# Kernel optimization log

Measured on AMD Instinct MI355X. Metric: run time of the kernel, lower is better.

## Reference

```python
import jax, jax.numpy as jnp
import numpy as np

B, C, N, T = 32, 32, 300, 64      # batch, residual/conv channels, nodes, seq_len
DIM, K, SKIP, GD = 40, 20, 64, 2  # node_dim, top-k (subgraph_size), skip_channels, gcn_depth
TANH_A, PROP_A = 3.0, 0.05
KSET = (2, 3, 6, 7)
TOUT = T - (KSET[-1] - 1)          # 58: time length after dilated inception (dilation=1)


def conv2d(x, w, b):
    y = jax.lax.conv_general_dilated(x, w, (1, 1), 'VALID', dimension_numbers=('NCHW', 'OIHW', 'NCHW'))
    return y + b[None, :, None, None]


def setup_inputs() -> dict:
    key = jax.random.key(0)
    ks = iter(jax.random.split(key, 48))
    def nrm(shape, s=1.0):
        return jax.random.normal(next(ks), shape, jnp.float32) * s
    inp = {
        'x': nrm((B, C, N, T)),
        'x_skip': nrm((B, SKIP, N, 1)),
        'idx': jnp.arange(N, dtype=jnp.int32),
        'emb1': nrm((N, DIM), 0.1), 'emb2': nrm((N, DIM), 0.1),
        'lin1_w': nrm((DIM, DIM), 0.15), 'lin1_b': jnp.zeros((DIM,), jnp.float32),
        'lin2_w': nrm((DIM, DIM), 0.15), 'lin2_b': jnp.zeros((DIM,), jnp.float32),
        'skip_w': nrm((SKIP, C, 1, TOUT), 0.05), 'skip_b': jnp.zeros((SKIP,), jnp.float32),
        'mp1_w': nrm((C, (GD + 1) * C, 1, 1), 0.1), 'mp1_b': jnp.zeros((C,), jnp.float32),
        'mp2_w': nrm((C, (GD + 1) * C, 1, 1), 0.1), 'mp2_b': jnp.zeros((C,), jnp.float32),
        'ln_w': jnp.ones((C, N, TOUT), jnp.float32), 'ln_b': jnp.zeros((C, N, TOUT), jnp.float32),
    }
    for k in KSET:
        inp[f'fw{k}'] = nrm((C // 4, C, 1, k), 0.1); inp[f'fb{k}'] = jnp.zeros((C // 4,), jnp.float32)
        inp[f'gw{k}'] = nrm((C // 4, C, 1, k), 0.1); inp[f'gb{k}'] = jnp.zeros((C // 4,), jnp.float32)
    return inp


def _forward(x, x_skip, idx, emb1, emb2, lin1_w, lin1_b, lin2_w, lin2_b,
             fws, gws, skip_w, skip_b, mp1_w, mp1_b, mp2_w, mp2_b, ln_w, ln_b):
    # --- GraphConstructor: learned sparse adjacency via tanh/relu/top-k/scatter ---
    n1 = jnp.tanh(TANH_A * (emb1[idx] @ lin1_w.T + lin1_b))
    n2 = jnp.tanh(TANH_A * (emb2[idx] @ lin2_w.T + lin2_b))
    a = n1 @ n2.T - n2 @ n1.T
    A = jax.nn.relu(jnp.tanh(TANH_A * a))
    _, cols = jax.lax.top_k(A, K)                               # [N, K] per-row top-k indices
    mask = jnp.zeros_like(A).at[jnp.arange(N)[:, None], cols].set(1.0)
    A = A * mask
    # --- DilatedInception filter/gate (Conv2d kernel (1,k), crop to shortest) ---
    Xf = jnp.tanh(jnp.concatenate([conv2d(x, w, b)[..., -TOUT:] for w, b in fws], axis=1))
    Xg = jax.nn.sigmoid(jnp.concatenate([conv2d(x, w, b)[..., -TOUT:] for w, b in gws], axis=1))
    X = Xf * Xg                                                 # dropout is identity (training=False)
    X_skip_out = conv2d(X, skip_w, skip_b) + x_skip             # [B, SKIP, N, 1]
    # --- MixProp graph diffusion over A and A^T ---
    def mixprop(Xin, Adj, w, b):
        Ah = Adj + jnp.eye(N, dtype=Adj.dtype)
        Ah = Ah / Ah.sum(1)[:, None]                            # row-normalize
        H, hops = Xin, [Xin]
        for _ in range(GD):
            H = PROP_A * Xin + (1.0 - PROP_A) * jnp.einsum('bcwt,vw->bcvt', H, Ah)
            hops.append(H)
        return conv2d(jnp.concatenate(hops, axis=1), w, b)      # 1x1 conv: (GD+1)*C -> C
    X = mixprop(X, A, mp1_w, mp1_b) + mixprop(X, A.T, mp2_w, mp2_b)
    X = X + x[..., -TOUT:]
    # --- LayerNorm over (C, N, TOUT) with node-indexed affine ---
    mu = X.mean(axis=(1, 2, 3), keepdims=True)
    var = ((X - mu) ** 2).mean(axis=(1, 2, 3), keepdims=True)
    Xn = (X - mu) * jax.lax.rsqrt(var + 1e-5)
    X = Xn * ln_w[:, idx, :][None] + ln_b[:, idx, :][None]
    return X, X_skip_out


def reference(x, x_skip, idx, emb1, emb2, lin1_w, lin1_b, lin2_w, lin2_b,
              fw2, fb2, fw3, fb3, fw6, fb6, fw7, fb7,
              gw2, gb2, gw3, gb3, gw6, gb6, gw7, gb7,
              skip_w, skip_b, mp1_w, mp1_b, mp2_w, mp2_b, ln_w, ln_b):
    fws = [(fw2, fb2), (fw3, fb3), (fw6, fb6), (fw7, fb7)]
    gws = [(gw2, gb2), (gw3, gb3), (gw6, gb6), (gw7, gb7)]
    return _forward(x, x_skip, idx, emb1, emb2, lin1_w, lin1_b, lin2_w, lin2_b,
                    fws, gws, skip_w, skip_b, mp1_w, mp1_b, mp2_w, mp2_b, ln_w, ln_b)
```

## Files before the change

kernel.cpp:

```cpp
#include <hip/hip_runtime.h>
#include <hip/hip_bf16.h>
#include <math.h>

typedef __hip_bfloat16 bf16;
typedef __attribute__((ext_vector_type(8))) short bf16x8;
typedef __attribute__((ext_vector_type(4))) float f32x4;

#define NB 32
#define NC 32
#define NNODE 300
#define NT 64
#define NDIM 40
#define KTOP 20
#define NSKIP 64
#define NTOUT 58
#define SLAB 17400
#define BSLAB 556800
#define XEL 17817600
#define PSLAB 2048
#define BPSLAB 614400
#define XPEL 19660800

__device__ __forceinline__ float b2f(bf16 v){ return __bfloat162float(v); }
__device__ __forceinline__ bf16 f2b(float v){ return __float2bfloat16(v); }
__device__ __forceinline__ float fsig(float x){ return 1.0f/(1.0f + __expf(-x)); }
__device__ __forceinline__ float ftanh(float x){ return 2.0f*fsig(2.0f*x) - 1.0f; }

__device__ __forceinline__ unsigned short bbits(float v){
  bf16 h = f2b(v); unsigned short s; __builtin_memcpy(&s, &h, 2); return s;
}

__device__ __forceinline__ void fma8(float acc[8], uint4 d, float vv){
  acc[0] = fmaf(vv, __uint_as_float(d.x << 16),          acc[0]);
  acc[1] = fmaf(vv, __uint_as_float(d.x & 0xffff0000u),  acc[1]);
  acc[2] = fmaf(vv, __uint_as_float(d.y << 16),          acc[2]);
  acc[3] = fmaf(vv, __uint_as_float(d.y & 0xffff0000u),  acc[3]);
  acc[4] = fmaf(vv, __uint_as_float(d.z << 16),          acc[4]);
  acc[5] = fmaf(vv, __uint_as_float(d.z & 0xffff0000u),  acc[5]);
  acc[6] = fmaf(vv, __uint_as_float(d.w << 16),          acc[6]);
  acc[7] = fmaf(vv, __uint_as_float(d.w & 0xffff0000u),  acc[7]);
}

__device__ __forceinline__ void unp8(float f[8], uint4 d){
  f[0] = __uint_as_float(d.x << 16); f[1] = __uint_as_float(d.x & 0xffff0000u);
  f[2] = __uint_as_float(d.y << 16); f[3] = __uint_as_float(d.y & 0xffff0000u);
  f[4] = __uint_as_float(d.z << 16); f[5] = __uint_as_float(d.z & 0xffff0000u);
  f[6] = __uint_as_float(d.w << 16); f[7] = __uint_as_float(d.w & 0xffff0000u);
}

__device__ __forceinline__ uint4 pack8(const float f[8]){
  uint4 d;
  d.x = (unsigned)bbits(f[0]) | ((unsigned)bbits(f[1]) << 16);
  d.y = (unsigned)bbits(f[2]) | ((unsigned)bbits(f[3]) << 16);
  d.z = (unsigned)bbits(f[4]) | ((unsigned)bbits(f[5]) << 16);
  d.w = (unsigned)bbits(f[6]) | ((unsigned)bbits(f[7]) << 16);
  return d;
}

__device__ __forceinline__ void bv_swz(int bid, int& b, int& v){
  int xcd = bid & 7, i = bid >> 3;
  int nb = xcd*1200 + i;
  b = nb / NNODE; v = nb - b*NNODE;
}

__global__ void k_nodes(const float* __restrict__ emb1, const float* __restrict__ emb2,
                        const float* __restrict__ l1w, const float* __restrict__ l1b,
                        const float* __restrict__ l2w, const float* __restrict__ l2b,
                        const int* __restrict__ idxp,
                        float* __restrict__ n1, float* __restrict__ n2){
  int i = blockIdx.x; int d = threadIdx.x;
  if (d >= NDIM) return;
  int r = idxp[i];
  float a1 = l1b[d], a2 = l2b[d];
  for (int k=0;k<NDIM;++k){
    a1 = fmaf(emb1[r*NDIM+k], l1w[d*NDIM+k], a1);
    a2 = fmaf(emb2[r*NDIM+k], l2w[d*NDIM+k], a2);
  }
  n1[i*NDIM+d] = tanhf(3.0f*a1);
  n2[i*NDIM+d] = tanhf(3.0f*a2);
}

__global__ void __launch_bounds__(64) k_adjrow(const float* __restrict__ n1,
                                               const float* __restrict__ n2,
                                               float* __restrict__ Am){
  int i = blockIdx.x; int lane = threadIdx.x;
  __shared__ float rowo[NNODE];
  __shared__ float rowv[NNODE];
  __shared__ int   sel[NNODE];
  for (int j=lane;j<NNODE;j+=64){
    float a = 0.f;
    #pragma unroll
    for (int k=0;k<NDIM;++k){
      float a1 = n1[i*NDIM+k], a2 = n2[i*NDIM+k];
      a = fmaf(a1, n2[j*NDIM+k], a);
      a = fmaf(-a2, n1[j*NDIM+k], a);
    }
    float v = tanhf(3.0f*a);
    v = v > 0.f ? v : 0.f;
    rowo[j]=v; rowv[j]=v; sel[j]=0;
  }
  __syncthreads();
  for (int it=0; it<KTOP; ++it){
    float best = -1.f; int bi = 0x7fffffff;
    for (int j=lane;j<NNODE;j+=64){
      float v = rowv[j];
      if (v > best){ best=v; bi=j; }
    }
    #pragma unroll
    for (int off=32; off; off>>=1){
      float ov = __shfl_xor(best, off);
      int   oi = __shfl_xor(bi, off);
      if (ov > best || (ov == best && oi < bi)){ best=ov; bi=oi; }
    }
    if (lane==0){ sel[bi]=1; rowv[bi]=-2.f; }
    __syncthreads();
  }
  for (int j=lane;j<NNODE;j+=64)
    Am[i*NNODE+j] = sel[j] ? rowo[j] : 0.f;
}

__global__ void __launch_bounds__(64) k_csr(const float* __restrict__ Am,
                                            int* __restrict__ aidx, float* __restrict__ aval,
                                            int* __restrict__ acnt){
  int r = blockIdx.x; int lane = threadIdx.x;
  int v = (r < NNODE) ? r : r - NNODE;
  int*   ip = aidx + r*304;
  float* vp = aval + r*304;
  if (lane==0){ ip[0]=v; vp[0]=1.0f; }
  int cnt = 1; float s = 1.0f;
  for (int base=0; base<NNODE; base+=64){
    int j = base + lane; float val = 0.f; bool p = false;
    if (j < NNODE){
      val = (r < NNODE) ? Am[v*NNODE + j] : Am[j*NNODE + v];
      p = val > 0.f;
    }
    unsigned long long m = __ballot(p);
    int pre = __popcll(m & ((1ull << lane) - 1ull));
    if (p){ ip[cnt+pre]=j; vp[cnt+pre]=val; }
    cnt += __popcll(m);
    float vs = p ? val : 0.f;
    #pragma unroll
    for (int off=32; off; off>>=1) vs += __shfl_xor(vs, off);
    s += vs;
  }
  for (int e=lane; e<cnt; e+=64) vp[e] = vp[e] / s;
  if (lane==0) acnt[r]=cnt;
}

__global__ void k_wpack2(const float* __restrict__ fw2,const float* __restrict__ fw3,
                         const float* __restrict__ fw6,const float* __restrict__ fw7,
                         const float* __restrict__ gw2,const float* __restrict__ gw3,
                         const float* __restrict__ gw6,const float* __restrict__ gw7,
                         const float* __restrict__ fb2,const float* __restrict__ fb3,
                         const float* __restrict__ fb6,const float* __restrict__ fb7,
                         const float* __restrict__ gb2,const float* __restrict__ gb3,
                         const float* __restrict__ gb6,const float* __restrict__ gb7,
                         bf16* __restrict__ wfA, float* __restrict__ biasPk){
  int T = blockIdx.x*blockDim.x + threadIdx.x;
  if (T < 14336){
    int j = T & 7;
    int q = T >> 3;
    int l = q & 63; q >>= 6;
    int ks = q % 7, mt = q / 7;
    int m = mt*16 + (l & 15);
    int k = ks*32 + (l >> 4)*8 + j;
    int c = m >> 1, path = m & 1;
    int cls = c >> 3, o = c & 7;
    int ic = k / 7, d = k - ic*7;
    int kk = (cls==0) ? 2 : (cls==1) ? 3 : (cls==2) ? 6 : 7;
    int tp = d - (7 - kk);
    float val = 0.f;
    if (tp >= 0){
      const float* w = (path==0)
        ? (cls==0?fw2:cls==1?fw3:cls==2?fw6:fw7)
        : (cls==0?gw2:cls==1?gw3:cls==2?gw6:gw7);
      val = w[(o*NC + ic)*kk + tp];
    }
    wfA[T] = f2b(val);
  } else if (T < 14336 + 32){
    int c = T - 14336;
    int cls = c >> 3, o = c & 7;
    const float* fb = cls==0?fb2:cls==1?fb3:cls==2?fb6:fb7;
    const float* gb = cls==0?gb2:cls==1?gb3:cls==2?gb6:gb7;
    biasPk[c*2]   = fb[o];
    biasPk[c*2+1] = gb[o];
  }
}

__global__ void k_wprepM(const float* __restrict__ m1w, const float* __restrict__ m2w,
                         const float* __restrict__ m1b, const float* __restrict__ m2b,
                         bf16* __restrict__ pkB0, bf16* __restrict__ pkB1,
                         float* __restrict__ biasSum){
  int id = blockIdx.x*blockDim.x + threadIdx.x;
  if (id < 3072){
    int j = id & 7, l = (id >> 3) & 63, q = id >> 9;
    int ks = q % 3, nt = q / 3;
    int k = ks*32 + (l >> 4)*8 + j;
    int c = nt*16 + (l & 15);
    float val = m1w[c*96 + k] + (k < 32 ? m2w[c*96 + k] : 0.f);
    pkB0[id] = f2b(val);
  } else if (id < 5120){
    int id2 = id - 3072;
    int j = id2 & 7, l = (id2 >> 3) & 63, q = id2 >> 9;
    int ks = q & 1, nt = q >> 1;
    int k = ks*32 + (l >> 4)*8 + j;
    int c = nt*16 + (l & 15);
    pkB1[id2] = f2b(m2w[c*96 + 32 + k]);
  } else if (id < 5152){
    int c = id - 5120;
    biasSum[c] = m1b[c] + m2b[c];
  }
}

__global__ void k_wTb(const float* __restrict__ sw, bf16* __restrict__ wTb){
  int id = blockIdx.x*blockDim.x + threadIdx.x;
  if (id >= 131072) return;
  int j = id & 7, l = (id >> 3) & 63, q = id >> 9;
  int ks = q & 63, nt = q >> 6;
  int k = ks*32 + (l >> 4)*8 + j;
  int t = k >> 5, c = k & 31;
  int sc = nt*16 + (l & 15);
  float val = (t < NTOUT) ? sw[sc*1856 + c*NTOUT + t] : 0.f;
  wTb[id] = f2b(val);
}

__global__ void __launch_bounds__(256) k_incepM(const float* __restrict__ x,
    const bf16* __restrict__ wfA, const float* __restrict__ biasPk,
    bf16* __restrict__ Xp){
  __shared__ bf16 xsb[32*72];
  __shared__ uint4 xim2[28*64];
  int b, n; bv_swz(blockIdx.x, b, n);
  int bn = b*NNODE + n;
  int tid = threadIdx.x;
  {
    int c = tid >> 3, t0 = (tid & 7)*8;
    const float* src = x + ((size_t)(b*NC + c)*NNODE + n)*NT + t0;
    float4 v0 = *reinterpret_cast<const float4*>(src);
    float4 v1 = *reinterpret_cast<const float4*>(src + 4);
    float f[8] = {v0.x,v0.y,v0.z,v0.w,v1.x,v1.y,v1.z,v1.w};
    *reinterpret_cast<uint4*>(&xsb[c*72 + t0]) = pack8(f);
    if ((tid & 7) == 7)
      *reinterpret_cast<uint4*>(&xsb[c*72 + 64]) = make_uint4(0,0,0,0);
  }
  __syncthreads();
  #pragma unroll
  for (int i=0;i<7;++i){
    int pr = tid + i*256;
    int kb = pr >> 6, t = pr & 63;
    int k0 = kb*8;
    int ic = k0 / 7, d = k0 - ic*7;
    unsigned sh[8];
    #pragma unroll
    for (int j=0;j<8;++j){
      sh[j] = *reinterpret_cast<const unsigned short*>(&xsb[ic*72 + t + d]);
      ++d; if (d == 7){ d = 0; ++ic; }
    }
    xim2[kb*64 + t] = make_uint4(sh[0]|(sh[1]<<16), sh[2]|(sh[3]<<16),
                                 sh[4]|(sh[5]<<16), sh[6]|(sh[7]<<16));
  }
  __syncthreads();
  int lane = tid & 63;
  int mt = __builtin_amdgcn_readfirstlane(tid >> 6);
  bf16x8 wA[7];
  #pragma unroll
  for (int ks=0; ks<7; ++ks)
    wA[ks] = *reinterpret_cast<const bf16x8*>(wfA + (size_t)((mt*7 + ks)*64 + lane)*8);
  int g = lane >> 4;
  int c0 = mt*8 + 2*g;
  float4 bias2 = *reinterpret_cast<const float4*>(biasPk + c0*2);
  #pragma unroll
  for (int nt=0; nt<4; ++nt){
    int t = (lane & 15) + nt*16;
    f32x4 acc = {0.f, 0.f, 0.f, 0.f};
    #pragma unroll
    for (int ks=0; ks<7; ++ks){
      bf16x8 bfr = __builtin_bit_cast(bf16x8, xim2[(ks*4 + g)*64 + t]);
      acc = __builtin_amdgcn_mfma_f32_16x16x32_bf16(wA[ks], bfr, acc, 0, 0, 0);
    }
    bool act = t < NTOUT;
    float X0 = act ? (ftanh(acc[0] + bias2.x) * fsig(acc[1] + bias2.y)) : 0.f;
    float X1 = act ? (ftanh(acc[2] + bias2.z) * fsig(acc[3] + bias2.w)) : 0.f;
    unsigned pv = (unsigned)bbits(X0) | ((unsigned)bbits(X1) << 16);
    *reinterpret_cast<unsigned*>(Xp + (size_t)bn*PSLAB + t*32 + c0) = pv;
  }
}

__global__ void __launch_bounds__(256) k_skipM(const bf16* __restrict__ Xp, const bf16* __restrict__ wTb,
      const float* __restrict__ skip_b, const float* __restrict__ x_skip, float* __restrict__ out){
  int bn0 = blockIdx.x * 16;
  int tid = threadIdx.x, lane = tid & 63;
  int nt = __builtin_amdgcn_readfirstlane(tid >> 6);
  int g = lane >> 4, col = lane & 15;
  const bf16* aptr = Xp + (size_t)(bn0 + col)*PSLAB + g*8;
  const bf16* bptr = wTb + ((size_t)nt*64*64 + lane)*8;
  f32x4 acc = {0.f, 0.f, 0.f, 0.f};
  #pragma unroll 4
  for (int ks=0; ks<64; ++ks){
    bf16x8 aF = *reinterpret_cast<const bf16x8*>(aptr + ks*32);
    bf16x8 bF = *reinterpret_cast<const bf16x8*>(bptr + (size_t)ks*512);
    acc = __builtin_amdgcn_mfma_f32_16x16x32_bf16(aF, bF, acc, 0, 0, 0);
  }
  int sc = nt*16 + col;
  float sb = skip_b[sc];
  #pragma unroll
  for (int r=0;r<4;++r){
    int bn = bn0 + g*4 + r;
    int b = bn / NNODE, n = bn - b*NNODE;
    size_t so = (size_t)b*NSKIP*NNODE + (size_t)sc*NNODE + n;
    out[(size_t)XEL + so] = acc[r] + sb + x_skip[so];
  }
}

__global__ void __launch_bounds__(256) k_prop(const bf16* __restrict__ Xp, bf16* __restrict__ HA,
    const int* __restrict__ aidx, const float* __restrict__ aval, const int* __restrict__ acnt,
    int rowoff){
  __shared__ int   sidx[304];
  __shared__ float sval[304];
  int b, v; bv_swz(blockIdx.x, b, v);
  int r = rowoff + v;
  int cnt = acnt[r];
  for (int e = threadIdx.x; e < cnt; e += 256){
    sidx[e] = aidx[r*304 + e] * PSLAB;
    sval[e] = aval[r*304 + e];
  }
  __syncthreads();
  int t = threadIdx.x >> 2, cb = threadIdx.x & 3;
  int off = t*32 + cb*8;
  const bf16* base = Xp + (size_t)b*BPSLAB + off;
  float acc[8] = {0,0,0,0,0,0,0,0};
  #pragma unroll 2
  for (int j=0;j<cnt;++j){
    uint4 d = *reinterpret_cast<const uint4*>(base + sidx[j]);
    fma8(acc, d, sval[j]);
  }
  size_t own = (size_t)b*BPSLAB + (size_t)v*PSLAB + off;
  uint4 dx = *reinterpret_cast<const uint4*>(Xp + own);
  float xf[8]; unp8(xf, dx);
  float h[8];
  #pragma unroll
  for (int k=0;k<8;++k) h[k] = fmaf(0.95f, acc[k], 0.05f*xf[k]);
  *reinterpret_cast<uint4*>(HA + own) = pack8(h);
}

__global__ void __launch_bounds__(256) k_fuse(const bf16* __restrict__ Xp, const bf16* __restrict__ HA,
    float* __restrict__ out, const float* __restrict__ x,
    const int* __restrict__ aidx, const float* __restrict__ aval, const int* __restrict__ acnt,
    const bf16* __restrict__ pkB, const float* __restrict__ biasSum,
    int rowoff, int side){
  __shared__ int   sidx[304];
  __shared__ float sval[304];
  __shared__ uint4 h2T4[256];
  int b, v; bv_swz(blockIdx.x, b, v);
  int r = rowoff + v;
  int cnt = acnt[r];
  for (int e = threadIdx.x; e < cnt; e += 256){
    sidx[e] = aidx[r*304 + e] * PSLAB;
    sval[e] = aval[r*304 + e];
  }
  __syncthreads();
  int tid = threadIdx.x;
  size_t bbase = (size_t)b*BPSLAB;
  size_t vbase = bbase + (size_t)v*PSLAB;
  {
    int t = tid >> 2, cb = tid & 3;
    int off = t*32 + cb*8;
    const bf16* base = HA + bbase + off;
    float acc[8] = {0,0,0,0,0,0,0,0};
    #pragma unroll 2
    for (int j=0;j<cnt;++j){
      uint4 d = *reinterpret_cast<const uint4*>(base + sidx[j]);
      fma8(acc, d, sval[j]);
    }
    uint4 dx = *reinterpret_cast<const uint4*>(Xp + vbase + off);
    float xf[8]; unp8(xf, dx);
    float h[8];
    #pragma unroll
    for (int k=0;k<8;++k) h[k] = fmaf(0.95f, acc[k], 0.05f*xf[k]);
    h2T4[t*4 + cb] = pack8(h);
  }
  __syncthreads();
  int lane = tid & 63;
  int mt = __builtin_amdgcn_readfirstlane(tid >> 6);
  int g = lane >> 4, col = lane & 15;
  int tRow = mt*16 + col;
  const bf16x8* h2p = reinterpret_cast<const bf16x8*>(h2T4);
  bf16x8 aF0, aF1, aF2;
  if (side == 0){
    aF0 = *reinterpret_cast<const bf16x8*>(Xp + vbase + tRow*32 + g*8);
    aF1 = *reinterpret_cast<const bf16x8*>(HA + vbase + tRow*32 + g*8);
    aF2 = h2p[tRow*4 + g];
  } else {
    aF0 = *reinterpret_cast<const bf16x8*>(HA + vbase + tRow*32 + g*8);
    aF1 = h2p[tRow*4 + g];
    aF2 = aF1;
  }
  int t0 = mt*16 + g*4;
  #pragma unroll
  for (int nt=0; nt<2; ++nt){
    int c_out = nt*16 + col;
    f32x4 acc;
    if (side == 0){
      float bv = biasSum[c_out];
      acc = (f32x4){bv, bv, bv, bv};
      bf16x8 w0 = *reinterpret_cast<const bf16x8*>(pkB + (size_t)((nt*3+0)*64 + lane)*8);
      bf16x8 w1 = *reinterpret_cast<const bf16x8*>(pkB + (size_t)((nt*3+1)*64 + lane)*8);
      bf16x8 w2 = *reinterpret_cast<const bf16x8*>(pkB + (size_t)((nt*3+2)*64 + lane)*8);
      acc = __builtin_amdgcn_mfma_f32_16x16x32_bf16(aF0, w0, acc, 0, 0, 0);
      acc = __builtin_amdgcn_mfma_f32_16x16x32_bf16(aF1, w1, acc, 0, 0, 0);
      acc = __builtin_amdgcn_mfma_f32_16x16x32_bf16(aF2, w2, acc, 0, 0, 0);
      float* po = out + ((size_t)(b*NC + c_out)*NNODE + v)*NTOUT + t0;
      if (t0 <= 54){
        *reinterpret_cast<float2*>(po)     = make_float2(acc[0], acc[1]);
        *reinterpret_cast<float2*>(po + 2) = make_float2(acc[2], acc[3]);
      } else if (t0 == 56){
        *reinterpret_cast<float2*>(po)     = make_float2(acc[0], acc[1]);
      }
    } else {
      acc = (f32x4){0.f, 0.f, 0.f, 0.f};
      bf16x8 w0 = *reinterpret_cast<const bf16x8*>(pkB + (size_t)((nt*2+0)*64 + lane)*8);
      bf16x8 w1 = *reinterpret_cast<const bf16x8*>(pkB + (size_t)((nt*2+1)*64 + lane)*8);
      acc = __builtin_amdgcn_mfma_f32_16x16x32_bf16(aF0, w0, acc, 0, 0, 0);
      acc = __builtin_amdgcn_mfma_f32_16x16x32_bf16(aF1, w1, acc, 0, 0, 0);
      float* po = out + ((size_t)(b*NC + c_out)*NNODE + v)*NTOUT + t0;
      const float* rx = x + ((size_t)(b*NC + c_out)*NNODE + v)*NT + 6 + t0;
      if (t0 <= 54){
        float2 o0 = *reinterpret_cast<const float2*>(po);
        float2 o1 = *reinterpret_cast<const float2*>(po + 2);
        float2 r0 = *reinterpret_cast<const float2*>(rx);
        float2 r1 = *reinterpret_cast<const float2*>(rx + 2);
        *reinterpret_cast<float2*>(po)     = make_float2(o0.x + acc[0] + r0.x, o0.y + acc[1] + r0.y);
        *reinterpret_cast<float2*>(po + 2) = make_float2(o1.x + acc[2] + r1.x, o1.y + acc[3] + r1.y);
      } else if (t0 == 56){
        float2 o0 = *reinterpret_cast<const float2*>(po);
        float2 r0 = *reinterpret_cast<const float2*>(rx);
        *reinterpret_cast<float2*>(po)     = make_float2(o0.x + acc[0] + r0.x, o0.y + acc[1] + r0.y);
      }
    }
  }
}

__global__ void __launch_bounds__(256) k_lnstat(const float* __restrict__ out, double* __restrict__ part){
  int blk = blockIdx.x; int b = blk >> 3, seg = blk & 7;
  const float* p = out + (size_t)b*BSLAB;
  int start = seg*69600, end = start + 69600;
  double s = 0.0, s2 = 0.0;
  for (int i = start + threadIdx.x; i < end; i += 256){
    double v = (double)p[i]; s += v; s2 += v*v;
  }
  #pragma unroll
  for (int off=32; off; off>>=1){ s += __shfl_down(s, off); s2 += __shfl_down(s2, off); }
  __shared__ double ls[4], ls2[4];
  int lane = threadIdx.x & 63, w = threadIdx.x >> 6;
  if (lane==0){ ls[w]=s; ls2[w]=s2; }
  __syncthreads();
  if (threadIdx.x==0){
    double a=0.0, a2=0.0;
    for (int i=0;i<4;++i){ a+=ls[i]; a2+=ls2[i]; }
    part[blk*2]=a; part[blk*2+1]=a2;
  }
}

__global__ void k_lnfin(const double* __restrict__ part, float* __restrict__ stats){
  int b = threadIdx.x; if (b >= 32) return;
  double s=0.0, s2=0.0;
  for (int seg=0; seg<8; ++seg){ s += part[(b*8+seg)*2]; s2 += part[(b*8+seg)*2+1]; }
  double n = (double)BSLAB;
  double mean = s/n;
  double var = s2/n - mean*mean;
  stats[b*2]   = (float)mean;
  stats[b*2+1] = (float)(1.0/sqrt(var + 1e-5));
}

__global__ void __launch_bounds__(256) k_lnapply(float* __restrict__ out, const float* __restrict__ stats,
        const float* __restrict__ lnw, const float* __restrict__ lnb, const int* __restrict__ idxp){
  int o = blockIdx.x*256 + threadIdx.x;
  int t = o % NTOUT; int v = (o / NTOUT) % NNODE; int c = (o / SLAB) % NC; int b = o / BSLAB;
  float mean = stats[b*2], rstd = stats[b*2+1];
  int vn = idxp[v];
  float wv = lnw[((size_t)c*NNODE + vn)*NTOUT + t];
  float bv = lnb[((size_t)c*NNODE + vn)*NTOUT + t];
  float vx = out[o];
  out[o] = (vx - mean)*rstd*wv + bv;
}

extern "C" void kernel_launch(void* const* d_in, const int* in_sizes, int n_in,
                              void* d_out, int out_size, void* d_ws, size_t ws_size,
                              hipStream_t stream) {
  (void)in_sizes; (void)n_in; (void)out_size; (void)ws_size;
  const float* x     = (const float*)d_in[0];
  const float* xskip = (const float*)d_in[1];
  const int*   idxp  = (const int*)d_in[2];
  const float* emb1  = (const float*)d_in[3];
  const float* emb2  = (const float*)d_in[4];
  const float* l1w   = (const float*)d_in[5];
  const float* l1b   = (const float*)d_in[6];
  const float* l2w   = (const float*)d_in[7];
  const float* l2b   = (const float*)d_in[8];
  const float* skw   = (const float*)d_in[9];
  const float* skb   = (const float*)d_in[10];
  const float* m1w   = (const float*)d_in[11];
  const float* m1b   = (const float*)d_in[12];
  const float* m2w   = (const float*)d_in[13];
  const float* m2b   = (const float*)d_in[14];
  const float* lnw   = (const float*)d_in[15];
  const float* lnb   = (const float*)d_in[16];
  const float* fw2=(const float*)d_in[17]; const float* fb2=(const float*)d_in[18];
  const float* gw2=(const float*)d_in[19]; const float* gb2=(const float*)d_in[20];
  const float* fw3=(const float*)d_in[21]; const float* fb3=(const float*)d_in[22];
  const float* gw3=(const float*)d_in[23]; const float* gb3=(const float*)d_in[24];
  const float* fw6=(const float*)d_in[25]; const float* fb6=(const float*)d_in[26];
  const float* gw6=(const float*)d_in[27]; const float* gb6=(const float*)d_in[28];
  const float* fw7=(const float*)d_in[29]; const float* fb7=(const float*)d_in[30];
  const float* gw7=(const float*)d_in[31]; const float* gb7=(const float*)d_in[32];
  float* out = (float*)d_out;

  char* wsbase = (char*)d_ws;
  size_t cur = 0;
  auto alloc = [&](size_t bytes)->char*{
    char* p = wsbase + cur;
    cur = (cur + bytes + 255) & ~(size_t)255;
    return p;
  };
  bf16*  Xp   = (bf16*) alloc((size_t)XPEL*2);
  bf16*  HA   = (bf16*) alloc((size_t)XPEL*2);
  float* n1   = (float*)alloc(12000*4);
  float* n2   = (float*)alloc(12000*4);
  float* Am   = (float*)alloc(90000*4);
  int*   aidx = (int*)  alloc(600*304*4);
  float* aval = (float*)alloc(600*304*4);
  int*   acnt = (int*)  alloc(600*4);
  bf16*  wTb  = (bf16*) alloc(131072*2);
  bf16*  wfA  = (bf16*) alloc(14336*2);
  float* biasPk = (float*)alloc(64*4);
  bf16*  pkB0 = (bf16*) alloc(3072*2);
  bf16*  pkB1 = (bf16*) alloc(2048*2);
  float* biasSum = (float*)alloc(32*4);
  double* part = (double*)alloc(256*2*8);
  float* stats = (float*)alloc(64*4);

  k_nodes <<<NNODE, 64, 0, stream>>>(emb1, emb2, l1w, l1b, l2w, l2b, idxp, n1, n2);
  k_adjrow<<<NNODE, 64, 0, stream>>>(n1, n2, Am);
  k_csr   <<<2*NNODE, 64, 0, stream>>>(Am, aidx, aval, acnt);

  k_wpack2<<<57, 256, 0, stream>>>(fw2,fw3,fw6,fw7, gw2,gw3,gw6,gw7,
                                   fb2,fb3,fb6,fb7, gb2,gb3,gb6,gb7, wfA, biasPk);
  k_wprepM<<<21, 256, 0, stream>>>(m1w, m2w, m1b, m2b, pkB0, pkB1, biasSum);
  k_wTb   <<<512, 256, 0, stream>>>(skw, wTb);

  k_incepM<<<NB*NNODE, 256, 0, stream>>>(x, wfA, biasPk, Xp);

  k_skipM<<<(NB*NNODE)/16, 256, 0, stream>>>(Xp, wTb, skb, xskip, out);

  k_prop<<<NB*NNODE, 256, 0, stream>>>(Xp, HA, aidx, aval, acnt, 0);
  k_fuse<<<NB*NNODE, 256, 0, stream>>>(Xp, HA, out, x, aidx, aval, acnt, pkB0, biasSum, 0, 0);

  k_prop<<<NB*NNODE, 256, 0, stream>>>(Xp, HA, aidx, aval, acnt, NNODE);
  k_fuse<<<NB*NNODE, 256, 0, stream>>>(Xp, HA, out, x, aidx, aval, acnt, pkB1, biasSum, NNODE, 1);

  k_lnstat<<<256, 256, 0, stream>>>(out, part);
  k_lnfin<<<1, 32, 0, stream>>>(part, stats);
  k_lnapply<<<XEL/256, 256, 0, stream>>>(out, stats, lnw, lnb, idxp);
}
```

Measured before the change: 454.6 us.

## Merge both mixprop sides into one prop launch and one fused MFMA epilogue

Runs the first-hop propagation for A and A^T in a single k_prop launch writing to separate HA buffers, with an XCD-aware block mapping. A single k_fuse kernel then does the second hop for both sides, stages X and all hops in padded shared memory, and applies a combined 5-slice MFMA 1x1 conv with a repacked weight buffer. The output is written once, which removes the read-modify-write of out and two kernel launches. In exchange it needs an extra HA buffer, more shared memory per block, and doubles the gather work inside each fuse block.

```diff
diff --git a/kernel.cpp b/kernel.cpp
--- a/kernel.cpp
+++ b/kernel.cpp
@@ -189,23 +189,20 @@
 
 __global__ void k_wprepM(const float* __restrict__ m1w, const float* __restrict__ m2w,
                          const float* __restrict__ m1b, const float* __restrict__ m2b,
-                         bf16* __restrict__ pkB0, bf16* __restrict__ pkB1,
-                         float* __restrict__ biasSum){
+                         bf16* __restrict__ pkB, float* __restrict__ biasSum){
   int id = blockIdx.x*blockDim.x + threadIdx.x;
-  if (id < 3072){
+  if (id < 5120){
     int j = id & 7, l = (id >> 3) & 63, q = id >> 9;
-    int ks = q % 3, nt = q / 3;
-    int k = ks*32 + (l >> 4)*8 + j;
+    int ks = q % 5, nt = q / 5;
+    int k = (l >> 4)*8 + j;
     int c = nt*16 + (l & 15);
-    float val = m1w[c*96 + k] + (k < 32 ? m2w[c*96 + k] : 0.f);
-    pkB0[id] = f2b(val);
-  } else if (id < 5120){
-    int id2 = id - 3072;
-    int j = id2 & 7, l = (id2 >> 3) & 63, q = id2 >> 9;
-    int ks = q & 1, nt = q >> 1;
-    int k = ks*32 + (l >> 4)*8 + j;
-    int c = nt*16 + (l & 15);
-    pkB1[id2] = f2b(m2w[c*96 + 32 + k]);
+    float val;
+    if      (ks == 0) val = m1w[c*96 + k] + m2w[c*96 + k];
+    else if (ks == 1) val = m1w[c*96 + 32 + k];
+    else if (ks == 2) val = m1w[c*96 + 64 + k];
+    else if (ks == 3) val = m2w[c*96 + 32 + k];
+    else              val = m2w[c*96 + 64 + k];
+    pkB[id] = f2b(val);
   } else if (id < 5152){
     int c = id - 5120;
     biasSum[c] = m1b[c] + m2b[c];
@@ -311,13 +308,18 @@
   }
 }
 
-__global__ void __launch_bounds__(256) k_prop(const bf16* __restrict__ Xp, bf16* __restrict__ HA,
-    const int* __restrict__ aidx, const float* __restrict__ aval, const int* __restrict__ acnt,
-    int rowoff){
+__global__ void __launch_bounds__(256) k_prop(const bf16* __restrict__ Xp,
+    bf16* __restrict__ HA0, bf16* __restrict__ HA1,
+    const int* __restrict__ aidx, const float* __restrict__ aval, const int* __restrict__ acnt){
   __shared__ int   sidx[304];
   __shared__ float sval[304];
-  int b, v; bv_swz(blockIdx.x, b, v);
-  int r = rowoff + v;
+  int bid = blockIdx.x;
+  int xcd = bid & 7, i = bid >> 3;
+  int side = i & 1, jj = i >> 1;
+  int nb = xcd*1200 + jj;
+  int b = nb / NNODE, v = nb - b*NNODE;
+  int r = (side ? NNODE : 0) + v;
+  bf16* HA = side ? HA1 : HA0;
   int cnt = acnt[r];
   for (int e = threadIdx.x; e < cnt; e += 256){
     sidx[e] = aidx[r*304 + e] * PSLAB;
@@ -328,7 +330,7 @@
   int off = t*32 + cb*8;
   const bf16* base = Xp + (size_t)b*BPSLAB + off;
   float acc[8] = {0,0,0,0,0,0,0,0};
-  #pragma unroll 2
+  #pragma unroll 4
   for (int j=0;j<cnt;++j){
     uint4 d = *reinterpret_cast<const uint4*>(base + sidx[j]);
     fma8(acc, d, sval[j]);
@@ -342,99 +344,106 @@
   *reinterpret_cast<uint4*>(HA + own) = pack8(h);
 }
 
-__global__ void __launch_bounds__(256) k_fuse(const bf16* __restrict__ Xp, const bf16* __restrict__ HA,
+__global__ void __launch_bounds__(256) k_fuse(const bf16* __restrict__ Xp,
+    const bf16* __restrict__ HA0, const bf16* __restrict__ HA1,
     float* __restrict__ out, const float* __restrict__ x,
     const int* __restrict__ aidx, const float* __restrict__ aval, const int* __restrict__ acnt,
-    const bf16* __restrict__ pkB, const float* __restrict__ biasSum,
-    int rowoff, int side){
-  __shared__ int   sidx[304];
-  __shared__ float sval[304];
-  __shared__ uint4 h2T4[256];
+    const bf16* __restrict__ pkB, const float* __restrict__ biasSum){
+  __shared__ int   sidx0[304];
+  __shared__ float sval0[304];
+  __shared__ int   sidx1[304];
+  __shared__ float sval1[304];
+  __shared__ uint4 xs4[320];
+  __shared__ uint4 h1a4[320];
+  __shared__ uint4 h2a4[320];
+  __shared__ uint4 h1b4[320];
+  __shared__ uint4 h2b4[320];
   int b, v; bv_swz(blockIdx.x, b, v);
-  int r = rowoff + v;
-  int cnt = acnt[r];
-  for (int e = threadIdx.x; e < cnt; e += 256){
-    sidx[e] = aidx[r*304 + e] * PSLAB;
-    sval[e] = aval[r*304 + e];
+  int r0 = v, r1 = NNODE + v;
+  int cnt0 = acnt[r0], cnt1 = acnt[r1];
+  for (int e = threadIdx.x; e < cnt0; e += 256){
+    sidx0[e] = aidx[r0*304 + e] * PSLAB;
+    sval0[e] = aval[r0*304 + e];
+  }
+  for (int e = threadIdx.x; e < cnt1; e += 256){
+    sidx1[e] = aidx[r1*304 + e] * PSLAB;
+    sval1[e] = aval[r1*304 + e];
   }
   __syncthreads();
   int tid = threadIdx.x;
+  int t = tid >> 2, cb = tid & 3;
+  int off = t*32 + cb*8;
+  int idx = t*5 + cb;
   size_t bbase = (size_t)b*BPSLAB;
   size_t vbase = bbase + (size_t)v*PSLAB;
+  uint4 dx = *reinterpret_cast<const uint4*>(Xp + vbase + off);
+  xs4[idx] = dx;
+  float xf[8]; unp8(xf, dx);
+  h1a4[idx] = *reinterpret_cast<const uint4*>(HA0 + vbase + off);
+  h1b4[idx] = *reinterpret_cast<const uint4*>(HA1 + vbase + off);
   {
-    int t = tid >> 2, cb = tid & 3;
-    int off = t*32 + cb*8;
-    const bf16* base = HA + bbase + off;
+    const bf16* base = HA0 + bbase + off;
     float acc[8] = {0,0,0,0,0,0,0,0};
-    #pragma unroll 2
-    for (int j=0;j<cnt;++j){
-      uint4 d = *reinterpret_cast<const uint4*>(base + sidx[j]);
-      fma8(acc, d, sval[j]);
-    }
-    uint4 dx = *reinterpret_cast<const uint4*>(Xp + vbase + off);
-    float xf[8]; unp8(xf, dx);
+    #pragma unroll 4
+    for (int j=0;j<cnt0;++j){
+      uint4 d = *reinterpret_cast<const uint4*>(base + sidx0[j]);
+      fma8(acc, d, sval0[j]);
+    }
     float h[8];
     #pragma unroll
     for (int k=0;k<8;++k) h[k] = fmaf(0.95f, acc[k], 0.05f*xf[k]);
-    h2T4[t*4 + cb] = pack8(h);
+    h2a4[idx] = pack8(h);
+  }
+  {
+    const bf16* base = HA1 + bbase + off;
+    float acc[8] = {0,0,0,0,0,0,0,0};
+    #pragma unroll 4
+    for (int j=0;j<cnt1;++j){
+      uint4 d = *reinterpret_cast<const uint4*>(base + sidx1[j]);
+      fma8(acc, d, sval1[j]);
+    }
+    float h[8];
+    #pragma unroll
+    for (int k=0;k<8;++k) h[k] = fmaf(0.95f, acc[k], 0.05f*xf[k]);
+    h2b4[idx] = pack8(h);
   }
   __syncthreads();
   int lane = tid & 63;
   int mt = __builtin_amdgcn_readfirstlane(tid >> 6);
   int g = lane >> 4, col = lane & 15;
   int tRow = mt*16 + col;
-  const bf16x8* h2p = reinterpret_cast<const bf16x8*>(h2T4);
-  bf16x8 aF0, aF1, aF2;
-  if (side == 0){
-    aF0 = *reinterpret_cast<const bf16x8*>(Xp + vbase + tRow*32 + g*8);
-    aF1 = *reinterpret_cast<const bf16x8*>(HA + vbase + tRow*32 + g*8);
-    aF2 = h2p[tRow*4 + g];
-  } else {
-    aF0 = *reinterpret_cast<const bf16x8*>(HA + vbase + tRow*32 + g*8);
-    aF1 = h2p[tRow*4 + g];
-    aF2 = aF1;
-  }
+  int fidx = tRow*5 + g;
+  bf16x8 aX  = __builtin_bit_cast(bf16x8, xs4[fidx]);
+  bf16x8 a1a = __builtin_bit_cast(bf16x8, h1a4[fidx]);
+  bf16x8 a2a = __builtin_bit_cast(bf16x8, h2a4[fidx]);
+  bf16x8 a1b = __builtin_bit_cast(bf16x8, h1b4[fidx]);
+  bf16x8 a2b = __builtin_bit_cast(bf16x8, h2b4[fidx]);
   int t0 = mt*16 + g*4;
   #pragma unroll
   for (int nt=0; nt<2; ++nt){
     int c_out = nt*16 + col;
-    f32x4 acc;
-    if (side == 0){
-      float bv = biasSum[c_out];
-      acc = (f32x4){bv, bv, bv, bv};
-      bf16x8 w0 = *reinterpret_cast<const bf16x8*>(pkB + (size_t)((nt*3+0)*64 + lane)*8);
-      bf16x8 w1 = *reinterpret_cast<const bf16x8*>(pkB + (size_t)((nt*3+1)*64 + lane)*8);
-      bf16x8 w2 = *reinterpret_cast<const bf16x8*>(pkB + (size_t)((nt*3+2)*64 + lane)*8);
-      acc = __builtin_amdgcn_mfma_f32_16x16x32_bf16(aF0, w0, acc, 0, 0, 0);
-      acc = __builtin_amdgcn_mfma_f32_16x16x32_bf16(aF1, w1, acc, 0, 0, 0);
-      acc = __builtin_amdgcn_mfma_f32_16x16x32_bf16(aF2, w2, acc, 0, 0, 0);
-      float* po = out + ((size_t)(b*NC + c_out)*NNODE + v)*NTOUT + t0;
-      if (t0 <= 54){
-        *reinterpret_cast<float2*>(po)     = make_float2(acc[0], acc[1]);
-        *reinterpret_cast<float2*>(po + 2) = make_float2(acc[2], acc[3]);
-      } else if (t0 == 56){
-        *reinterpret_cast<float2*>(po)     = make_float2(acc[0], acc[1]);
-      }
-    } else {
-      acc = (f32x4){0.f, 0.f, 0.f, 0.f};
-      bf16x8 w0 = *reinterpret_cast<const bf16x8*>(pkB + (size_t)((nt*2+0)*64 + lane)*8);
-      bf16x8 w1 = *reinterpret_cast<const bf16x8*>(pkB + (size_t)((nt*2+1)*64 + lane)*8);
-      acc = __builtin_amdgcn_mfma_f32_16x16x32_bf16(aF0, w0, acc, 0, 0, 0);
-      acc = __builtin_amdgcn_mfma_f32_16x16x32_bf16(aF1, w1, acc, 0, 0, 0);
-      float* po = out + ((size_t)(b*NC + c_out)*NNODE + v)*NTOUT + t0;
-      const float* rx = x + ((size_t)(b*NC + c_out)*NNODE + v)*NT + 6 + t0;
-      if (t0 <= 54){
-        float2 o0 = *reinterpret_cast<const float2*>(po);
-        float2 o1 = *reinterpret_cast<const float2*>(po + 2);
-        float2 r0 = *reinterpret_cast<const float2*>(rx);
-        float2 r1 = *reinterpret_cast<const float2*>(rx + 2);
-        *reinterpret_cast<float2*>(po)     = make_float2(o0.x + acc[0] + r0.x, o0.y + acc[1] + r0.y);
-        *reinterpret_cast<float2*>(po + 2) = make_float2(o1.x + acc[2] + r1.x, o1.y + acc[3] + r1.y);
-      } else if (t0 == 56){
-        float2 o0 = *reinterpret_cast<const float2*>(po);
-        float2 r0 = *reinterpret_cast<const float2*>(rx);
-        *reinterpret_cast<float2*>(po)     = make_float2(o0.x + acc[0] + r0.x, o0.y + acc[1] + r0.y);
-      }
+    float bv = biasSum[c_out];
+    f32x4 acc = {bv, bv, bv, bv};
+    bf16x8 w0 = *reinterpret_cast<const bf16x8*>(pkB + (size_t)((nt*5+0)*64 + lane)*8);
+    bf16x8 w1 = *reinterpret_cast<const bf16x8*>(pkB + (size_t)((nt*5+1)*64 + lane)*8);
+    bf16x8 w2 = *reinterpret_cast<const bf16x8*>(pkB + (size_t)((nt*5+2)*64 + lane)*8);
+    bf16x8 w3 = *reinterpret_cast<const bf16x8*>(pkB + (size_t)((nt*5+3)*64 + lane)*8);
+    bf16x8 w4 = *reinterpret_cast<const bf16x8*>(pkB + (size_t)((nt*5+4)*64 + lane)*8);
+    acc = __builtin_amdgcn_mfma_f32_16x16x32_bf16(aX,  w0, acc, 0, 0, 0);
+    acc = __builtin_amdgcn_mfma_f32_16x16x32_bf16(a1a, w1, acc, 0, 0, 0);
+    acc = __builtin_amdgcn_mfma_f32_16x16x32_bf16(a2a, w2, acc, 0, 0, 0);
+    acc = __builtin_amdgcn_mfma_f32_16x16x32_bf16(a1b, w3, acc, 0, 0, 0);
+    acc = __builtin_amdgcn_mfma_f32_16x16x32_bf16(a2b, w4, acc, 0, 0, 0);
+    float* po = out + ((size_t)(b*NC + c_out)*NNODE + v)*NTOUT + t0;
+    const float* rx = x + ((size_t)(b*NC + c_out)*NNODE + v)*NT + 6 + t0;
+    if (t0 <= 54){
+      float2 r0v = *reinterpret_cast<const float2*>(rx);
+      float2 r1v = *reinterpret_cast<const float2*>(rx + 2);
+      *reinterpret_cast<float2*>(po)     = make_float2(acc[0] + r0v.x, acc[1] + r0v.y);
+      *reinterpret_cast<float2*>(po + 2) = make_float2(acc[2] + r1v.x, acc[3] + r1v.y);
+    } else if (t0 == 56){
+      float2 r0v = *reinterpret_cast<const float2*>(rx);
+      *reinterpret_cast<float2*>(po)     = make_float2(acc[0] + r0v.x, acc[1] + r0v.y);
     }
   }
 }
@@ -522,7 +531,8 @@
     return p;
   };
   bf16*  Xp   = (bf16*) alloc((size_t)XPEL*2);
-  bf16*  HA   = (bf16*) alloc((size_t)XPEL*2);
+  bf16*  HA0  = (bf16*) alloc((size_t)XPEL*2);
+  bf16*  HA1  = (bf16*) alloc((size_t)XPEL*2);
   float* n1   = (float*)alloc(12000*4);
   float* n2   = (float*)alloc(12000*4);
   float* Am   = (float*)alloc(90000*4);
@@ -532,8 +542,7 @@
   bf16*  wTb  = (bf16*) alloc(131072*2);
   bf16*  wfA  = (bf16*) alloc(14336*2);
   float* biasPk = (float*)alloc(64*4);
-  bf16*  pkB0 = (bf16*) alloc(3072*2);
-  bf16*  pkB1 = (bf16*) alloc(2048*2);
+  bf16*  pkB  = (bf16*) alloc(5120*2);
   float* biasSum = (float*)alloc(32*4);
   double* part = (double*)alloc(256*2*8);
   float* stats = (float*)alloc(64*4);
@@ -544,18 +553,16 @@
 
   k_wpack2<<<57, 256, 0, stream>>>(fw2,fw3,fw6,fw7, gw2,gw3,gw6,gw7,
                                    fb2,fb3,fb6,fb7, gb2,gb3,gb6,gb7, wfA, biasPk);
-  k_wprepM<<<21, 256, 0, stream>>>(m1w, m2w, m1b, m2b, pkB0, pkB1, biasSum);
+  k_wprepM<<<21, 256, 0, stream>>>(m1w, m2w, m1b, m2b, pkB, biasSum);
   k_wTb   <<<512, 256, 0, stream>>>(skw, wTb);
 
   k_incepM<<<NB*NNODE, 256, 0, stream>>>(x, wfA, biasPk, Xp);
 
   k_skipM<<<(NB*NNODE)/16, 256, 0, stream>>>(Xp, wTb, skb, xskip, out);
 
-  k_prop<<<NB*NNODE, 256, 0, stream>>>(Xp, HA, aidx, aval, acnt, 0);
-  k_fuse<<<NB*NNODE, 256, 0, stream>>>(Xp, HA, out, x, aidx, aval, acnt, pkB0, biasSum, 0, 0);
-
-  k_prop<<<NB*NNODE, 256, 0, stream>>>(Xp, HA, aidx, aval, acnt, NNODE);
-  k_fuse<<<NB*NNODE, 256, 0, stream>>>(Xp, HA, out, x, aidx, aval, acnt, pkB1, biasSum, NNODE, 1);
+  k_prop<<<2*NB*NNODE, 256, 0, stream>>>(Xp, HA0, HA1, aidx, aval, acnt);
+
+  k_fuse<<<NB*NNODE, 256, 0, stream>>>(Xp, HA0, HA1, out, x, aidx, aval, acnt, pkB, biasSum);
 
   k_lnstat<<<256, 256, 0, stream>>>(out, part);
   k_lnfin<<<1, 32, 0, stream>>>(part, stats);
```

Result: no change. 448.7 us (-1.3%).
